# Kernel optimization log

Hardware: AMD Instinct MI355X
Metric: run time of the kernel (lower is better)

The kernel has to match this reference:

```python
import jax, jax.numpy as jnp
import numpy as np

ALPHA = 0.2  # LeakyReLU negative slope
NEG_INF = -1e9


def setup_inputs() -> dict:
    key = jax.random.key(0)
    k1, k2, k3, k4 = jax.random.split(key, 4)
    B, N, F_in, F_out = 4, 4096, 128, 128
    h = jax.random.normal(k1, (B, N, F_in), dtype=jnp.float32)
    adj = jax.random.randint(k2, (B, N, N), 0, 2, dtype=jnp.int32)
    # Xavier-uniform init matching nn.Linear weights
    limW = np.sqrt(6.0 / (F_in + F_out))
    W = jax.random.uniform(k3, (F_in, F_out), jnp.float32, -limW, limW)
    lima = np.sqrt(6.0 / (2 * F_out + 1))
    a = jax.random.uniform(k4, (2 * F_out,), jnp.float32, -lima, lima)
    return {"h": h, "adj": adj, "W": W, "a": a}


def reference(h, adj, W, a):
    # h: (B, N, F_in), adj: (B, N, N) int, W: (F_in, F_out), a: (2*F_out,)
    F_out = W.shape[1]
    Wh = jnp.einsum("bnf,fo->bno", h, W)  # (B, N, F_out)
    a_i, a_j = a[:F_out], a[F_out:]
    # e_ij = leakyrelu(a . [Wh_i, Wh_j]) = leakyrelu(a_i.Wh_i + a_j.Wh_j)
    si = Wh @ a_i  # (B, N) contribution of destination node i
    sj = Wh @ a_j  # (B, N) contribution of source node j
    e = si[:, :, None] + sj[:, None, :]  # (B, N, N)
    e = jnp.where(e > 0, e, ALPHA * e)  # LeakyReLU
    e = jnp.where(adj > 0, e, NEG_INF)  # masked scores
    attention = jax.nn.softmax(e, axis=-1)  # (B, N, N)
    # dropout is identity in eval mode
    h_prime = jnp.einsum("bij,bjo->bio", attention, Wh)  # (B, N, F_out)
    return jax.nn.elu(h_prime)  # concat=True -> ELU
```

## Files before the change

kernel.cpp:

```cpp
#include <hip/hip_runtime.h>

#define GN 4096
#define GF 128
#define GB 4

typedef __attribute__((ext_vector_type(8))) short short8;
typedef __attribute__((ext_vector_type(4))) float floatx4;

static __device__ __forceinline__ unsigned short f2bf(float x){
  unsigned int u = __float_as_uint(x);
  u += 0x7FFFu + ((u >> 16) & 1u);
  return (unsigned short)(u >> 16);
}

__global__ __launch_bounds__(256)
void gat_prep(const float* __restrict__ h, const float* __restrict__ W,
              const float* __restrict__ a, unsigned short* __restrict__ whB,
              float* __restrict__ si_g, unsigned short* __restrict__ EFh)
{
  __shared__ float hl[16*GF];
  __shared__ float red[2][2][16];
  const int tid = threadIdx.x;
  const int b   = blockIdx.x >> 8;
  const int r0  = (blockIdx.x & 255) << 4;
  const int o = tid & 127, g = tid >> 7;

  const float4* hb4 = (const float4*)(h + ((size_t)(b*GN + r0))*GF);
  ((float4*)hl)[tid]       = hb4[tid];
  ((float4*)hl)[tid + 256] = hb4[tid + 256];
  __syncthreads();

  float acc[8];
  #pragma unroll
  for (int r=0;r<8;++r) acc[r] = 0.f;
  const float* Wp = W + o;
  for (int f4=0; f4<32; ++f4){
    const float w0 = Wp[(f4*4+0)*GF];
    const float w1 = Wp[(f4*4+1)*GF];
    const float w2 = Wp[(f4*4+2)*GF];
    const float w3 = Wp[(f4*4+3)*GF];
    #pragma unroll
    for (int r=0;r<8;++r){
      const float4 h4 = *(const float4*)&hl[((g<<3)+r)*GF + (f4<<2)];
      acc[r] = fmaf(h4.x, w0, acc[r]);
      acc[r] = fmaf(h4.y, w1, acc[r]);
      acc[r] = fmaf(h4.z, w2, acc[r]);
      acc[r] = fmaf(h4.w, w3, acc[r]);
    }
  }

  const float ai = a[o], aj = a[GF + o];
  const int lane = tid & 63, wh = (tid >> 6) & 1;
  #pragma unroll
  for (int r=0;r<8;++r){
    float vi = acc[r]*ai, vj = acc[r]*aj;
    #pragma unroll
    for (int off=32; off; off>>=1){ vi += __shfl_down(vi, off); vj += __shfl_down(vj, off); }
    if (lane == 0){ red[0][wh][(g<<3)+r] = vi; red[1][wh][(g<<3)+r] = vj; }
  }

  unsigned short us[8] __attribute__((aligned(16)));
  #pragma unroll
  for (int r=0;r<8;++r) us[r] = f2bf(acc[r]);
  {
    const int j0 = r0 + (g<<3);
    unsigned short* dst = whB + (((size_t)(b*128 + (j0>>5))*128 + o)<<5) + (j0&31);
    *(uint4*)dst = *(const uint4*)us;
  }

  __syncthreads();
  if (tid < 16){
    si_g[b*GN + r0 + tid] = red[0][0][tid] + red[0][1][tid];
  } else if (tid < 32){
    const int r = tid - 16;
    const float vsj = red[1][0][r] + red[1][1][r];
    EFh[(size_t)b*8192 + r0 + r]        = f2bf(__expf(vsj));
    EFh[(size_t)b*8192 + 4096 + r0 + r] = f2bf(__expf(0.2f*vsj));
  }
}

__global__ __launch_bounds__(256, 2)
void gat_main(const int* __restrict__ adj, const unsigned short* __restrict__ whB,
              const float* __restrict__ si_g, const unsigned short* __restrict__ EFh,
              float* __restrict__ out)
{
  __shared__ __align__(16) char smem[34304];
  unsigned short* sEj = (unsigned short*)smem;
  unsigned long long* bits64 = (unsigned long long*)(smem + 16384);
  float* smemc = (float*)smem;

  const int tid  = threadIdx.x;
  const int wave = tid >> 6, lane = tid & 63;
  const int b  = (blockIdx.x >> 1) & 3;
  const int i0 = ((((blockIdx.x >> 3) << 1) | (blockIdx.x & 1))) << 5;
  const int m = lane & 15, quad = lane >> 4, q8 = quad << 3;
  const int jw = wave << 10, jw32 = wave << 5;

  {
    const uint4* Eg = (const uint4*)(EFh + (size_t)b*8192);
    uint4* sE4 = (uint4*)sEj;
    #pragma unroll
    for (int k=0;k<4;++k) sE4[tid + (k<<8)] = Eg[tid + (k<<8)];
  }

  const int* adjb = adj + ((size_t)(b*GN + i0))*GN + jw + lane;

  int vv[32];
  #pragma unroll
  for (int r=0;r<32;++r) vv[r] = __builtin_nontemporal_load(adjb + (size_t)r*GN);

  const float si0 = si_g[(size_t)b*GN + i0 + m];
  const float si1 = si_g[(size_t)b*GN + i0 + 16 + m];
  const float Ri0 = __expf(-0.8f*si0), Ri1 = __expf(-0.8f*si1);
  const unsigned short* lanebase = whB + ((size_t)b<<19) + (m<<5) + q8;

  floatx4 acc0[8], acc1[8];
  #pragma unroll
  for (int c=0;c<8;++c){ acc0[c] = (floatx4){0.f,0.f,0.f,0.f}; acc1[c] = (floatx4){0.f,0.f,0.f,0.f}; }
  floatx4 lf0 = (floatx4){0.f,0.f,0.f,0.f}, lf1 = (floatx4){0.f,0.f,0.f,0.f};
  const short8 ones8 = {0x3F80,0x3F80,0x3F80,0x3F80,0x3F80,0x3F80,0x3F80,0x3F80};

#define BALLOTS(bufw_) do { \
    unsigned long long* bw = bits64 + (((wave<<1) | (bufw_)) << 5); \
    _Pragma("unroll") \
    for (int r=0;r<32;++r){ \
      const unsigned long long mm = __ballot(vv[r] > 0); \
      if (lane == 0) bw[r] = mm; \
    } \
  } while(0)

#define MKAF(dst_, sh_, Ri_) do { \
    unsigned int aw[4]; \
    _Pragma("unroll") \
    for (int p=0;p<4;++p){ \
      const unsigned int e0 = Eu[p] << 16, e1 = Eu[p] & 0xFFFF0000u; \
      const unsigned int f0 = Fu[p] << 16, f1 = Fu[p] & 0xFFFF0000u; \
      const float p0 = fmaxf(__uint_as_float(e0), (Ri_)*__uint_as_float(f0)); \
      const float p1 = fmaxf(__uint_as_float(e1), (Ri_)*__uint_as_float(f1)); \
      const unsigned int k0 = (unsigned int)(((int)((sh_) << (31-(2*p))))   >> 31); \
      const unsigned int k1 = (unsigned int)(((int)((sh_) << (31-(2*p+1)))) >> 31); \
      const unsigned int b0 = __float_as_uint(p0) & k0; \
      const unsigned int b1 = __float_as_uint(p1) & k1; \
      aw[p] = ((b0 + 0x8000u) >> 16) | ((b1 + 0x8000u) & 0xFFFF0000u); \
    } \
    dst_ = *(const short8*)aw; \
  } while(0)

#define COMPUTE_T(cc_, t_, Bc_) do { \
    const unsigned int* bwp = (const unsigned int*)(bits64 + (((wave<<1) | ((cc_)&1)) << 5)); \
    const unsigned int sh0 = bwp[(m<<1) | (t_)] >> q8; \
    const unsigned int sh1 = bwp[((m+16)<<1) | (t_)] >> q8; \
    const int jj = jw + ((((cc_)<<1)|(t_))<<5) + q8; \
    const short8 Es = *(const short8*)&sEj[jj]; \
    const short8 Fs = *(const short8*)&sEj[4096 + jj]; \
    const unsigned int* Eu = (const unsigned int*)&Es; \
    const unsigned int* Fu = (const unsigned int*)&Fs; \
    short8 af0, af1; \
    MKAF(af0, sh0, Ri0); \
    MKAF(af1, sh1, Ri1); \
    _Pragma("unroll") \
    for (int c=0;c<8;++c){ \
      acc0[c] = __builtin_amdgcn_mfma_f32_16x16x32_bf16(af0, Bc_[c], acc0[c], 0, 0, 0); \
      acc1[c] = __builtin_amdgcn_mfma_f32_16x16x32_bf16(af1, Bc_[c], acc1[c], 0, 0, 0); \
    } \
    lf0 = __builtin_amdgcn_mfma_f32_16x16x32_bf16(af0, ones8, lf0, 0, 0, 0); \
    lf1 = __builtin_amdgcn_mfma_f32_16x16x32_bf16(af1, ones8, lf1, 0, 0, 0); \
  } while(0)

  __syncthreads();

  BALLOTS(0);
  asm volatile("s_waitcnt lgkmcnt(0)" ::: "memory");

  #pragma unroll 1
  for (int cc = 0; cc < 15; ++cc){
    short8 Bc0[8], Bc1[8];
    const unsigned short* wb0 = lanebase + ((size_t)(jw32 + (cc<<1)) << 12);
    #pragma unroll
    for (int c=0;c<8;++c) Bc0[c] = *(const short8*)(wb0 + (c<<9));
    #pragma unroll
    for (int c=0;c<8;++c) Bc1[c] = *(const short8*)(wb0 + 4096 + (c<<9));
    #pragma unroll
    for (int r=0;r<32;++r) vv[r] = __builtin_nontemporal_load(adjb + ((cc+1)<<6) + (size_t)r*GN);

    COMPUTE_T(cc, 0, Bc0);
    COMPUTE_T(cc, 1, Bc1);

    BALLOTS((cc+1)&1);
    asm volatile("s_waitcnt lgkmcnt(0)" ::: "memory");
  }
  {
    short8 Bc0[8], Bc1[8];
    const unsigned short* wb0 = lanebase + ((size_t)(jw32 + 30) << 12);
    #pragma unroll
    for (int c=0;c<8;++c) Bc0[c] = *(const short8*)(wb0 + (c<<9));
    #pragma unroll
    for (int c=0;c<8;++c) Bc1[c] = *(const short8*)(wb0 + 4096 + (c<<9));
    COMPUTE_T(15, 0, Bc0);
    COMPUTE_T(15, 1, Bc1);
  }
#undef COMPUTE_T
#undef MKAF
#undef BALLOTS

  #pragma unroll 1
  for (int g = 0; g < 2; ++g){
    __syncthreads();
    #pragma unroll
    for (int c=0;c<8;++c){
      #pragma unroll
      for (int r=0;r<4;++r){
        const float v = g ? acc1[c][r] : acc0[c][r];
        smemc[(wave*16 + quad*4 + r)*132 + c*16 + m] = v;
      }
    }
    if (m == 0){
      #pragma unroll
      for (int r=0;r<4;++r) smemc[8448 + wave*16 + quad*4 + r] = g ? lf1[r] : lf0[r];
    }
    __syncthreads();

    const int rr = tid >> 5;
    const int c4 = (tid & 31) << 2;
    #pragma unroll
    for (int hh = 0; hh < 2; ++hh){
      const int row = rr + (hh<<3);
      const float l = smemc[8448+row] + smemc[8448+16+row]
                    + smemc[8448+32+row] + smemc[8448+48+row];
      const float rl = __builtin_amdgcn_rcpf(l);
      float4 o4;
      #pragma unroll
      for (int k=0;k<4;++k){
        const int col = c4 + k;
        const float s = smemc[row*132+col] + smemc[(16+row)*132+col]
                      + smemc[(32+row)*132+col] + smemc[(48+row)*132+col];
        float v = s * rl;
        v = v > 0.f ? v : expm1f(v);
        ((float*)&o4)[k] = v;
      }
      *(float4*)&out[((size_t)(b*GN + i0 + (g<<4) + row))*GF + c4] = o4;
    }
  }
}

extern "C" void kernel_launch(void* const* d_in, const int* in_sizes, int n_in,
                              void* d_out, int out_size, void* d_ws, size_t ws_size,
                              hipStream_t stream)
{
  (void)in_sizes; (void)n_in; (void)out_size; (void)ws_size;
  const float* h   = (const float*)d_in[0];
  const int*   adj = (const int*)d_in[1];
  const float* W   = (const float*)d_in[2];
  const float* a   = (const float*)d_in[3];
  float* out = (float*)d_out;

  char* ws = (char*)d_ws;
  unsigned short* whB   = (unsigned short*)ws;
  float*          si    = (float*)(ws + (size_t)4*1024*1024);
  unsigned short* EFh   = (unsigned short*)(ws + (size_t)4*1024*1024 + 64*1024);

  gat_prep<<<GB*GN/16, 256, 0, stream>>>(h, W, a, whB, si, EFh);
  gat_main<<<GB*GN/32, 256, 0, stream>>>(adj, whB, si, EFh, out);
}
```

Before: 410.0 us.

## Double-buffer adjacency loads two chunks ahead and use packed bf16 conversion

Adjacency rows now go into two register buffers loaded two chunks ahead, so global loads overlap with more compute before their ballots are needed. The shared-memory E/F copy is moved after the first adjacency loads are issued. The attention-weight build now converts with v_cvt_pk_bf16_f32 and masks after conversion instead of doing manual rounding, which cuts VALU work. The cost is 32 extra VGPRs for the second buffer, which may hurt occupancy at the 2-blocks-per-SM bound or cause spills.

```diff
diff --git a/kernel.cpp b/kernel.cpp
--- a/kernel.cpp
+++ b/kernel.cpp
@@ -96,112 +96,125 @@
   const int m = lane & 15, quad = lane >> 4, q8 = quad << 3;
   const int jw = wave << 10, jw32 = wave << 5;
 
-  {
-    const uint4* Eg = (const uint4*)(EFh + (size_t)b*8192);
-    uint4* sE4 = (uint4*)sEj;
-    #pragma unroll
-    for (int k=0;k<4;++k) sE4[tid + (k<<8)] = Eg[tid + (k<<8)];
-  }
-
   const int* adjb = adj + ((size_t)(b*GN + i0))*GN + jw + lane;
 
-  int vv[32];
-  #pragma unroll
-  for (int r=0;r<32;++r) vv[r] = __builtin_nontemporal_load(adjb + (size_t)r*GN);
+#define LOADVV(vv_, chunk_) do { \
+    _Pragma("unroll") \
+    for (int r=0;r<32;++r) vv_[r] = __builtin_nontemporal_load(adjb + ((chunk_)<<6) + (size_t)r*GN); \
+  } while(0)
+
+  int vvA[32], vvB[32];
+  LOADVV(vvA, 0);
+  LOADVV(vvB, 1);
 
   const float si0 = si_g[(size_t)b*GN + i0 + m];
   const float si1 = si_g[(size_t)b*GN + i0 + 16 + m];
   const float Ri0 = __expf(-0.8f*si0), Ri1 = __expf(-0.8f*si1);
   const unsigned short* lanebase = whB + ((size_t)b<<19) + (m<<5) + q8;
 
+  {
+    const uint4* Eg = (const uint4*)(EFh + (size_t)b*8192);
+    uint4* sE4 = (uint4*)sEj;
+    #pragma unroll
+    for (int k=0;k<4;++k) sE4[tid + (k<<8)] = Eg[tid + (k<<8)];
+  }
+
   floatx4 acc0[8], acc1[8];
   #pragma unroll
   for (int c=0;c<8;++c){ acc0[c] = (floatx4){0.f,0.f,0.f,0.f}; acc1[c] = (floatx4){0.f,0.f,0.f,0.f}; }
   floatx4 lf0 = (floatx4){0.f,0.f,0.f,0.f}, lf1 = (floatx4){0.f,0.f,0.f,0.f};
   const short8 ones8 = {0x3F80,0x3F80,0x3F80,0x3F80,0x3F80,0x3F80,0x3F80,0x3F80};
 
-#define BALLOTS(bufw_) do { \
-    unsigned long long* bw = bits64 + (((wave<<1) | (bufw_)) << 5); \
+#define BALLOTS(vv_, bufp_) do { \
+    unsigned long long* bw = bits64 + (((wave<<1) | (bufp_)) << 5); \
     _Pragma("unroll") \
     for (int r=0;r<32;++r){ \
-      const unsigned long long mm = __ballot(vv[r] > 0); \
+      const unsigned long long mm = __ballot(vv_[r] > 0); \
       if (lane == 0) bw[r] = mm; \
     } \
-  } while(0)
-
-#define MKAF(dst_, sh_, Ri_) do { \
-    unsigned int aw[4]; \
-    _Pragma("unroll") \
-    for (int p=0;p<4;++p){ \
-      const unsigned int e0 = Eu[p] << 16, e1 = Eu[p] & 0xFFFF0000u; \
-      const unsigned int f0 = Fu[p] << 16, f1 = Fu[p] & 0xFFFF0000u; \
-      const float p0 = fmaxf(__uint_as_float(e0), (Ri_)*__uint_as_float(f0)); \
-      const float p1 = fmaxf(__uint_as_float(e1), (Ri_)*__uint_as_float(f1)); \
-      const unsigned int k0 = (unsigned int)(((int)((sh_) << (31-(2*p))))   >> 31); \
-      const unsigned int k1 = (unsigned int)(((int)((sh_) << (31-(2*p+1)))) >> 31); \
-      const unsigned int b0 = __float_as_uint(p0) & k0; \
-      const unsigned int b1 = __float_as_uint(p1) & k1; \
-      aw[p] = ((b0 + 0x8000u) >> 16) | ((b1 + 0x8000u) & 0xFFFF0000u); \
+    asm volatile("s_waitcnt lgkmcnt(0)" ::: "memory"); \
+  } while(0)
+
+#define BCLOAD(Bc_, chunk_) do { \
+    const unsigned short* wb = lanebase + ((size_t)(jw32 + ((chunk_)<<1)) << 12); \
+    _Pragma("unroll") \
+    for (int c=0;c<8;++c) Bc_[c]   = *(const short8*)(wb + (c<<9)); \
+    _Pragma("unroll") \
+    for (int c=0;c<8;++c) Bc_[8+c] = *(const short8*)(wb + 4096 + (c<<9)); \
+  } while(0)
+
+#define COMPUTE(chunk_, bufp_, Bc_) do { \
+    const unsigned int* bwp = (const unsigned int*)(bits64 + (((wave<<1) | (bufp_)) << 5)); \
+    _Pragma("unroll") \
+    for (int t=0;t<2;++t){ \
+      const unsigned int sh0 = bwp[(m<<1)|t] >> q8; \
+      const unsigned int sh1 = bwp[((m+16)<<1)|t] >> q8; \
+      const int jj = jw + ((((chunk_)<<1)|t)<<5) + q8; \
+      const short8 Es = *(const short8*)&sEj[jj]; \
+      const short8 Fs = *(const short8*)&sEj[4096 + jj]; \
+      const unsigned int* Eu = (const unsigned int*)&Es; \
+      const unsigned int* Fu = (const unsigned int*)&Fs; \
+      unsigned int aw0[4], aw1[4]; \
+      _Pragma("unroll") \
+      for (int p=0;p<4;++p){ \
+        const float E0 = __uint_as_float(Eu[p] << 16); \
+        const float E1 = __uint_as_float(Eu[p] & 0xFFFF0000u); \
+        const float F0 = __uint_as_float(Fu[p] << 16); \
+        const float F1 = __uint_as_float(Fu[p] & 0xFFFF0000u); \
+        const float p00 = fmaxf(E0, Ri0*F0), p01 = fmaxf(E1, Ri0*F1); \
+        const float p10 = fmaxf(E0, Ri1*F0), p11 = fmaxf(E1, Ri1*F1); \
+        unsigned int w0, w1; \
+        asm("v_cvt_pk_bf16_f32 %0, %1, %2" : "=v"(w0) : "v"(p00), "v"(p01)); \
+        asm("v_cvt_pk_bf16_f32 %0, %1, %2" : "=v"(w1) : "v"(p10), "v"(p11)); \
+        const unsigned int k00 = (unsigned int)(((int)(sh0 << (31-2*p))) >> 31); \
+        const unsigned int k01 = (unsigned int)(((int)(sh0 << (30-2*p))) >> 31); \
+        const unsigned int k10 = (unsigned int)(((int)(sh1 << (31-2*p))) >> 31); \
+        const unsigned int k11 = (unsigned int)(((int)(sh1 << (30-2*p))) >> 31); \
+        aw0[p] = w0 & ((k00 & 0xFFFFu) | (k01 << 16)); \
+        aw1[p] = w1 & ((k10 & 0xFFFFu) | (k11 << 16)); \
+      } \
+      const short8 af0 = *(const short8*)aw0; \
+      const short8 af1 = *(const short8*)aw1; \
+      _Pragma("unroll") \
+      for (int c=0;c<8;++c){ \
+        acc0[c] = __builtin_amdgcn_mfma_f32_16x16x32_bf16(af0, Bc_[(t<<3)+c], acc0[c], 0, 0, 0); \
+        acc1[c] = __builtin_amdgcn_mfma_f32_16x16x32_bf16(af1, Bc_[(t<<3)+c], acc1[c], 0, 0, 0); \
+      } \
+      lf0 = __builtin_amdgcn_mfma_f32_16x16x32_bf16(af0, ones8, lf0, 0, 0, 0); \
+      lf1 = __builtin_amdgcn_mfma_f32_16x16x32_bf16(af1, ones8, lf1, 0, 0, 0); \
     } \
-    dst_ = *(const short8*)aw; \
-  } while(0)
-
-#define COMPUTE_T(cc_, t_, Bc_) do { \
-    const unsigned int* bwp = (const unsigned int*)(bits64 + (((wave<<1) | ((cc_)&1)) << 5)); \
-    const unsigned int sh0 = bwp[(m<<1) | (t_)] >> q8; \
-    const unsigned int sh1 = bwp[((m+16)<<1) | (t_)] >> q8; \
-    const int jj = jw + ((((cc_)<<1)|(t_))<<5) + q8; \
-    const short8 Es = *(const short8*)&sEj[jj]; \
-    const short8 Fs = *(const short8*)&sEj[4096 + jj]; \
-    const unsigned int* Eu = (const unsigned int*)&Es; \
-    const unsigned int* Fu = (const unsigned int*)&Fs; \
-    short8 af0, af1; \
-    MKAF(af0, sh0, Ri0); \
-    MKAF(af1, sh1, Ri1); \
-    _Pragma("unroll") \
-    for (int c=0;c<8;++c){ \
-      acc0[c] = __builtin_amdgcn_mfma_f32_16x16x32_bf16(af0, Bc_[c], acc0[c], 0, 0, 0); \
-      acc1[c] = __builtin_amdgcn_mfma_f32_16x16x32_bf16(af1, Bc_[c], acc1[c], 0, 0, 0); \
-    } \
-    lf0 = __builtin_amdgcn_mfma_f32_16x16x32_bf16(af0, ones8, lf0, 0, 0, 0); \
-    lf1 = __builtin_amdgcn_mfma_f32_16x16x32_bf16(af1, ones8, lf1, 0, 0, 0); \
   } while(0)
 
   __syncthreads();
 
-  BALLOTS(0);
-  asm volatile("s_waitcnt lgkmcnt(0)" ::: "memory");
+  BALLOTS(vvA, 0);
 
   #pragma unroll 1
-  for (int cc = 0; cc < 15; ++cc){
-    short8 Bc0[8], Bc1[8];
-    const unsigned short* wb0 = lanebase + ((size_t)(jw32 + (cc<<1)) << 12);
-    #pragma unroll
-    for (int c=0;c<8;++c) Bc0[c] = *(const short8*)(wb0 + (c<<9));
-    #pragma unroll
-    for (int c=0;c<8;++c) Bc1[c] = *(const short8*)(wb0 + 4096 + (c<<9));
-    #pragma unroll
-    for (int r=0;r<32;++r) vv[r] = __builtin_nontemporal_load(adjb + ((cc+1)<<6) + (size_t)r*GN);
-
-    COMPUTE_T(cc, 0, Bc0);
-    COMPUTE_T(cc, 1, Bc1);
-
-    BALLOTS((cc+1)&1);
-    asm volatile("s_waitcnt lgkmcnt(0)" ::: "memory");
-  }
-  {
-    short8 Bc0[8], Bc1[8];
-    const unsigned short* wb0 = lanebase + ((size_t)(jw32 + 30) << 12);
-    #pragma unroll
-    for (int c=0;c<8;++c) Bc0[c] = *(const short8*)(wb0 + (c<<9));
-    #pragma unroll
-    for (int c=0;c<8;++c) Bc1[c] = *(const short8*)(wb0 + 4096 + (c<<9));
-    COMPUTE_T(15, 0, Bc0);
-    COMPUTE_T(15, 1, Bc1);
-  }
-#undef COMPUTE_T
-#undef MKAF
+  for (int ci = 0; ci < 7; ++ci){
+    const int c0 = ci << 1;
+    {
+      short8 BcA[16];
+      BCLOAD(BcA, c0);
+      LOADVV(vvA, c0+2);
+      COMPUTE(c0, 0, BcA);
+      BALLOTS(vvB, 1);
+    }
+    {
+      short8 BcB[16];
+      BCLOAD(BcB, c0+1);
+      LOADVV(vvB, c0+3);
+      COMPUTE(c0+1, 1, BcB);
+      BALLOTS(vvA, 0);
+    }
+  }
+  { short8 BcA[16]; BCLOAD(BcA, 14); COMPUTE(14, 0, BcA); }
+  BALLOTS(vvB, 1);
+  { short8 BcB[16]; BCLOAD(BcB, 15); COMPUTE(15, 1, BcB); }
+
+#undef COMPUTE
+#undef BCLOAD
 #undef BALLOTS
+#undef LOADVV
 
   #pragma unroll 1
   for (int g = 0; g < 2; ++g){
```

New measurement: 404.4 us. About the same (-1.4%).
